# Performance work log

Hardware: AMD Instinct MI355X
Metric: run time of the kernel (lower is better)

Reference implementation:

```python
import math
import jax, jax.numpy as jnp
import numpy as np

K = 1048576  # number of spheres
M = 4        # num_vertices
D = M - 1    # 3
EPS = 1e-12


def _simplex_vertices(n):
    # get_n_simplex_coordinates(n): (n+1) unit vectors in R^n
    p = np.eye(n)
    a = (1.0 + math.sqrt(n + 1)) / n
    p = np.vstack([a * np.ones((1, n)), p])
    p = p - p.mean(axis=0, keepdims=True)
    p = p / np.linalg.norm(p, axis=1, keepdims=True)
    return p  # (n+1, n), float64


def _refl_np(S, u):
    # f(S, u) = S - 2 u (u^T S) / ||u||^2  (batched, numpy float64)
    v = np.einsum('bi,bij->bj', u, S) / (np.linalg.norm(u, axis=1, keepdims=True) ** 2)
    return S - 2.0 * u[:, :, None] * v[:, None, :]


def _rot_np(p, q):
    B, d = p.shape
    I = np.tile(np.eye(d)[None], (B, 1, 1))
    S = _refl_np(I, p + q)
    return _refl_np(S, q)


def setup_inputs() -> dict:
    verts = _simplex_vertices(D)  # (4, 3)
    tetra = [np.eye(D)] + [_rot_np(verts[0:1], verts[i:i + 1])[0] for i in range(1, M)]
    tetra = np.stack(tetra)  # (4, 3, 3)
    key = jax.random.key(0)
    spheres = jax.random.normal(key, (K, D + 2), dtype=jnp.float32)
    return {
        'spheres': spheres,
        'ones_vec': jnp.asarray(verts[0], jnp.float32),            # (3,)
        'tetra_rotations': jnp.asarray(tetra, jnp.float32),        # (4, 3, 3)
    }


def _reflection(S, u):
    v = jnp.einsum('bi,bij->bj', u, S) / jnp.sum(u * u, axis=1, keepdims=True)
    return S - 2.0 * u[:, :, None] * v[:, None, :]


def _rotation_from_two_points(p, q):
    B, d = p.shape
    I = jnp.broadcast_to(jnp.eye(d, dtype=p.dtype), (B, d, d))
    S = _reflection(I, p + q)
    return _reflection(S, q)


def _apply_rot_isom(points, rots):
    # isom = blockdiag(rot, I_2); apply to embedded points (B, D+2)
    top = jnp.einsum('bij,bj->bi', rots, points[:, :D])
    return jnp.concatenate([top, points[:, D:]], axis=-1)


def reference(spheres, ones_vec, tetra_rotations):
    # unembed: centers in R^D
    centers = spheres[:, :D] / (spheres[:, -1:] + EPS)
    centers_n = centers / jnp.linalg.norm(centers, axis=1, keepdims=True)
    ones = ones_vec / jnp.linalg.norm(ones_vec)
    ones_b = jnp.broadcast_to(ones[None, :], centers_n.shape)
    # R0 centers_n = ones
    rotations_0 = _rotation_from_two_points(centers_n, ones_b)  # (K, D, D)
    rotated_spheres = _apply_rot_isom(spheres, rotations_0)     # (K, D+2)
    # b = R0^T @ T_m for each (k, m); block-diag isom applied to rotated spheres
    b = jnp.einsum('kji,mjl->kmil', rotations_0, tetra_rotations)  # (K, M, D, D)
    fb_top = jnp.einsum('kmij,kj->kmi', b, rotated_spheres[:, :D])  # (K, M, D)
    fb_rest = jnp.broadcast_to(rotated_spheres[:, None, D:], (spheres.shape[0], M, 2))
    filter_banks = jnp.concatenate([fb_top, fb_rest], axis=-1).reshape(-1, D + 2, 1)  # (M*K, D+2, 1)
    return rotations_0, filter_banks
```

## Files before the change

kernel.cpp:

```cpp
#include <hip/hip_runtime.h>
#include <math.h>


typedef float vf4 __attribute__((ext_vector_type(4)));

__global__ __launch_bounds__(256) void fbank_kernel(
    const float* __restrict__ spheres,
    const float* __restrict__ ones_vec,
    const float* __restrict__ tetra,
    float* __restrict__ out,
    int K)
{
    __shared__ float sT[36];
    __shared__ __align__(16) float rot_s[256 * 9];
    __shared__ __align__(16) float u_s[256 * 21];

    const int tid = threadIdx.x;
    const size_t base  = (size_t)blockIdx.x * 1280;
    const size_t total = (size_t)K * 5;
    const bool full = (base + 1280 <= total);

    {
        const vf4* spv = (const vf4*)(spheres + base);
        if (full) {
            *(vf4*)&u_s[tid * 4] = spv[tid];
            if (tid < 64) *(vf4*)&u_s[(256 + tid) * 4] = spv[256 + tid];
        } else {
            for (int i = tid; i < 320; i += 256)
                if (base + (size_t)i * 4 + 4 <= total)
                    *(vf4*)&u_s[i * 4] = spv[i];
        }
    }
    if (tid < 36) sT[tid] = tetra[tid];
    __syncthreads();

    const float s0 = u_s[tid * 5 + 0], s1 = u_s[tid * 5 + 1], s2 = u_s[tid * 5 + 2];
    const float s3 = u_s[tid * 5 + 3], s4 = u_s[tid * 5 + 4];

    const float inv = __builtin_amdgcn_rcpf(s4 + 1e-12f);
    const float c0 = s0 * inv, c1 = s1 * inv, c2 = s2 * inv;
    const float rn = __builtin_amdgcn_rsqf(c0 * c0 + c1 * c1 + c2 * c2);
    const float p0 = c0 * rn, p1 = c1 * rn, p2 = c2 * rn;

    float o0 = ones_vec[0], o1 = ones_vec[1], o2 = ones_vec[2];
    const float orn = __builtin_amdgcn_rsqf(o0 * o0 + o1 * o1 + o2 * o2);
    o0 *= orn; o1 *= orn; o2 *= orn;

    const float u0 = p0 + o0, u1 = p1 + o1, u2 = p2 + o2;
    const float a  = 2.0f * __builtin_amdgcn_rcpf(u0 * u0 + u1 * u1 + u2 * u2);
    const float atq = a * (o0 * u0 + o1 * u1 + o2 * u2);
    const float w0 = o0 - atq * u0, w1 = o1 - atq * u1, w2 = o2 - atq * u2;

    const float uu[3] = {u0, u1, u2}, oo[3] = {o0, o1, o2}, ww[3] = {w0, w1, w2};
    float R[3][3];
#pragma unroll
    for (int i = 0; i < 3; ++i)
#pragma unroll
        for (int j = 0; j < 3; ++j)
            R[i][j] = ((i == j) ? 1.0f : 0.0f) - a * uu[i] * uu[j] - 2.0f * oo[i] * ww[j];

    const float r0 = R[0][0] * s0 + R[0][1] * s1 + R[0][2] * s2;
    const float r1 = R[1][0] * s0 + R[1][1] * s1 + R[1][2] * s2;
    const float r2 = R[2][0] * s0 + R[2][1] * s1 + R[2][2] * s2;

    float f[12];
#pragma unroll
    for (int m = 0; m < 4; ++m) {
        const float* T = sT + m * 9;
        const float g0 = T[0] * r0 + T[1] * r1 + T[2] * r2;
        const float g1 = T[3] * r0 + T[4] * r1 + T[5] * r2;
        const float g2 = T[6] * r0 + T[7] * r1 + T[8] * r2;
        f[m * 3 + 0] = R[0][0] * g0 + R[1][0] * g1 + R[2][0] * g2;
        f[m * 3 + 1] = R[0][1] * g0 + R[1][1] * g1 + R[2][1] * g2;
        f[m * 3 + 2] = R[0][2] * g0 + R[1][2] * g1 + R[2][2] * g2;
    }

    __syncthreads();

#pragma unroll
    for (int i = 0; i < 3; ++i)
#pragma unroll
        for (int j = 0; j < 3; ++j)
            rot_s[tid * 9 + i * 3 + j] = R[i][j];
#pragma unroll
    for (int m = 0; m < 4; ++m) {
        u_s[tid * 21 + m * 5 + 0] = f[m * 3 + 0];
        u_s[tid * 21 + m * 5 + 1] = f[m * 3 + 1];
        u_s[tid * 21 + m * 5 + 2] = f[m * 3 + 2];
        u_s[tid * 21 + m * 5 + 3] = s3;
        u_s[tid * 21 + m * 5 + 4] = s4;
    }
    __syncthreads();

    float* rot_out = out + (size_t)blockIdx.x * 2304;
    float* fb_out  = out + (size_t)K * 9 + (size_t)blockIdx.x * 5120;
    if (full) {
        for (int i = tid; i < 1856; i += 256) {
            if (i < 576) {
                *(vf4*)(rot_out + (size_t)i * 4) = *(const vf4*)&rot_s[i * 4];
            } else {
                const int fo = (i - 576) * 4;
                vf4 v;
                v.x = u_s[((fo + 0) / 20) * 21 + (fo + 0) % 20];
                v.y = u_s[((fo + 1) / 20) * 21 + (fo + 1) % 20];
                v.z = u_s[((fo + 2) / 20) * 21 + (fo + 2) % 20];
                v.w = u_s[((fo + 3) / 20) * 21 + (fo + 3) % 20];
                *(vf4*)(fb_out + fo) = v;
            }
        }
    } else {
        const long long limr = (long long)K * 9 - (long long)blockIdx.x * 2304;
        for (int i = tid; i < 576; i += 256)
            if ((long long)i * 4 + 3 < limr)
                *(vf4*)(rot_out + (size_t)i * 4) = *(const vf4*)&rot_s[i * 4];
        const long long limf = (long long)K * 20 - (long long)blockIdx.x * 5120;
        for (int i = tid; i < 1280; i += 256) {
            const int fo = i * 4;
            if ((long long)fo + 3 < limf) {
                vf4 v;
                v.x = u_s[((fo + 0) / 20) * 21 + (fo + 0) % 20];
                v.y = u_s[((fo + 1) / 20) * 21 + (fo + 1) % 20];
                v.z = u_s[((fo + 2) / 20) * 21 + (fo + 2) % 20];
                v.w = u_s[((fo + 3) / 20) * 21 + (fo + 3) % 20];
                *(vf4*)(fb_out + fo) = v;
            }
        }
    }
}

extern "C" void kernel_launch(void* const* d_in, const int* in_sizes, int n_in,
                              void* d_out, int out_size, void* d_ws, size_t ws_size,
                              hipStream_t stream) {
    const float* spheres  = (const float*)d_in[0];
    const float* ones_vec = (const float*)d_in[1];
    const float* tetra    = (const float*)d_in[2];
    float* out = (float*)d_out;
    const int K = in_sizes[0] / 5;
    const int grid = (K + 255) / 256;
    fbank_kernel<<<grid, 256, 0, stream>>>(spheres, ones_vec, tetra, out, K);
}
```

Measured before the change: 141.0 us.

## Use direct global-to-LDS loads, unpadded vf4 staging, and nontemporal stores

Input tiles are now loaded straight into LDS with global_load_lds, and one vf4 buffer is reused for both input and output staging. Each thread packs its 20 filter-bank floats into five vf4 words, so the strided, div/mod-indexed gather on the write-out path goes away. Output stores become nontemporal with a fixed per-thread layout, and the tetra matrices are read from global memory instead of shared memory. The costs are an extra barrier, a possible LDS bank conflict pattern from the 5-vf4 stride, and dependence on an intrinsic whose exact semantics are specific to the hardware.

```diff
diff --git a/kernel.cpp b/kernel.cpp
--- a/kernel.cpp
+++ b/kernel.cpp
@@ -11,31 +11,32 @@
     float* __restrict__ out,
     int K)
 {
-    __shared__ float sT[36];
     __shared__ __align__(16) float rot_s[256 * 9];
-    __shared__ __align__(16) float u_s[256 * 21];
+    __shared__ __align__(16) vf4   fb_s[256 * 5];
 
     const int tid = threadIdx.x;
     const size_t base  = (size_t)blockIdx.x * 1280;
     const size_t total = (size_t)K * 5;
     const bool full = (base + 1280 <= total);
 
-    {
+    if (full) {
+        __builtin_amdgcn_global_load_lds((const unsigned int*)(spheres + base) + tid * 4,
+                                         (unsigned int*)fb_s + tid * 4, 16, 0, 0);
+        if (tid < 64)
+            __builtin_amdgcn_global_load_lds((const unsigned int*)(spheres + base) + 1024 + tid * 4,
+                                             (unsigned int*)fb_s + 1024 + tid * 4, 16, 0, 0);
+    } else {
         const vf4* spv = (const vf4*)(spheres + base);
-        if (full) {
-            *(vf4*)&u_s[tid * 4] = spv[tid];
-            if (tid < 64) *(vf4*)&u_s[(256 + tid) * 4] = spv[256 + tid];
-        } else {
-            for (int i = tid; i < 320; i += 256)
-                if (base + (size_t)i * 4 + 4 <= total)
-                    *(vf4*)&u_s[i * 4] = spv[i];
-        }
+        for (int i = tid; i < 320; i += 256)
+            if (base + (size_t)i * 4 + 4 <= total)
+                fb_s[i] = spv[i];
     }
-    if (tid < 36) sT[tid] = tetra[tid];
     __syncthreads();
 
-    const float s0 = u_s[tid * 5 + 0], s1 = u_s[tid * 5 + 1], s2 = u_s[tid * 5 + 2];
-    const float s3 = u_s[tid * 5 + 3], s4 = u_s[tid * 5 + 4];
+    const float* inS = (const float*)fb_s;
+    const float s0 = inS[tid * 5 + 0], s1 = inS[tid * 5 + 1], s2 = inS[tid * 5 + 2];
+    const float s3 = inS[tid * 5 + 3], s4 = inS[tid * 5 + 4];
+    __syncthreads();
 
     const float inv = __builtin_amdgcn_rcpf(s4 + 1e-12f);
     const float c0 = s0 * inv, c1 = s1 * inv, c2 = s2 * inv;
@@ -59,6 +60,12 @@
         for (int j = 0; j < 3; ++j)
             R[i][j] = ((i == j) ? 1.0f : 0.0f) - a * uu[i] * uu[j] - 2.0f * oo[i] * ww[j];
 
+#pragma unroll
+    for (int i = 0; i < 3; ++i)
+#pragma unroll
+        for (int j = 0; j < 3; ++j)
+            rot_s[tid * 9 + i * 3 + j] = R[i][j];
+
     const float r0 = R[0][0] * s0 + R[0][1] * s1 + R[0][2] * s2;
     const float r1 = R[1][0] * s0 + R[1][1] * s1 + R[1][2] * s2;
     const float r2 = R[2][0] * s0 + R[2][1] * s1 + R[2][2] * s2;
@@ -66,7 +73,7 @@
     float f[12];
 #pragma unroll
     for (int m = 0; m < 4; ++m) {
-        const float* T = sT + m * 9;
+        const float* T = tetra + m * 9;
         const float g0 = T[0] * r0 + T[1] * r1 + T[2] * r2;
         const float g1 = T[3] * r0 + T[4] * r1 + T[5] * r2;
         const float g2 = T[6] * r0 + T[7] * r1 + T[8] * r2;
@@ -75,56 +82,43 @@
         f[m * 3 + 2] = R[0][2] * g0 + R[1][2] * g1 + R[2][2] * g2;
     }
 
-    __syncthreads();
-
-#pragma unroll
-    for (int i = 0; i < 3; ++i)
-#pragma unroll
-        for (int j = 0; j < 3; ++j)
-            rot_s[tid * 9 + i * 3 + j] = R[i][j];
-#pragma unroll
-    for (int m = 0; m < 4; ++m) {
-        u_s[tid * 21 + m * 5 + 0] = f[m * 3 + 0];
-        u_s[tid * 21 + m * 5 + 1] = f[m * 3 + 1];
-        u_s[tid * 21 + m * 5 + 2] = f[m * 3 + 2];
-        u_s[tid * 21 + m * 5 + 3] = s3;
-        u_s[tid * 21 + m * 5 + 4] = s4;
+    {
+        vf4 v0, v1, v2, v3, v4;
+        v0.x = f[0];  v0.y = f[1];  v0.z = f[2];  v0.w = s3;
+        v1.x = s4;    v1.y = f[3];  v1.z = f[4];  v1.w = f[5];
+        v2.x = s3;    v2.y = s4;    v2.z = f[6];  v2.w = f[7];
+        v3.x = f[8];  v3.y = s3;    v3.z = s4;    v3.w = f[9];
+        v4.x = f[10]; v4.y = f[11]; v4.z = s3;    v4.w = s4;
+        fb_s[tid * 5 + 0] = v0;
+        fb_s[tid * 5 + 1] = v1;
+        fb_s[tid * 5 + 2] = v2;
+        fb_s[tid * 5 + 3] = v3;
+        fb_s[tid * 5 + 4] = v4;
     }
     __syncthreads();
 
     float* rot_out = out + (size_t)blockIdx.x * 2304;
     float* fb_out  = out + (size_t)K * 9 + (size_t)blockIdx.x * 5120;
     if (full) {
-        for (int i = tid; i < 1856; i += 256) {
-            if (i < 576) {
-                *(vf4*)(rot_out + (size_t)i * 4) = *(const vf4*)&rot_s[i * 4];
-            } else {
-                const int fo = (i - 576) * 4;
-                vf4 v;
-                v.x = u_s[((fo + 0) / 20) * 21 + (fo + 0) % 20];
-                v.y = u_s[((fo + 1) / 20) * 21 + (fo + 1) % 20];
-                v.z = u_s[((fo + 2) / 20) * 21 + (fo + 2) % 20];
-                v.w = u_s[((fo + 3) / 20) * 21 + (fo + 3) % 20];
-                *(vf4*)(fb_out + fo) = v;
-            }
-        }
+        vf4* ro = (vf4*)rot_out;
+        const vf4* rs = (const vf4*)rot_s;
+        __builtin_nontemporal_store(rs[tid],       &ro[tid]);
+        __builtin_nontemporal_store(rs[256 + tid], &ro[256 + tid]);
+        if (tid < 64)
+            __builtin_nontemporal_store(rs[512 + tid], &ro[512 + tid]);
+        vf4* fo = (vf4*)fb_out;
+#pragma unroll
+        for (int j = 0; j < 5; ++j)
+            __builtin_nontemporal_store(fb_s[j * 256 + tid], &fo[j * 256 + tid]);
     } else {
         const long long limr = (long long)K * 9 - (long long)blockIdx.x * 2304;
         for (int i = tid; i < 576; i += 256)
             if ((long long)i * 4 + 3 < limr)
                 *(vf4*)(rot_out + (size_t)i * 4) = *(const vf4*)&rot_s[i * 4];
         const long long limf = (long long)K * 20 - (long long)blockIdx.x * 5120;
-        for (int i = tid; i < 1280; i += 256) {
-            const int fo = i * 4;
-            if ((long long)fo + 3 < limf) {
-                vf4 v;
-                v.x = u_s[((fo + 0) / 20) * 21 + (fo + 0) % 20];
-                v.y = u_s[((fo + 1) / 20) * 21 + (fo + 1) % 20];
-                v.z = u_s[((fo + 2) / 20) * 21 + (fo + 2) % 20];
-                v.w = u_s[((fo + 3) / 20) * 21 + (fo + 3) % 20];
-                *(vf4*)(fb_out + fo) = v;
-            }
-        }
+        for (int i = tid; i < 1280; i += 256)
+            if ((long long)i * 4 + 3 < limf)
+                *(vf4*)(fb_out + (size_t)i * 4) = fb_s[i];
     }
 }
 
```

Result: slower. 146.6 us (+4.0%).
